# Kernel tuning notes

Hardware: AMD Instinct MI355X
Metric: run time of the kernel (lower is better)

The kernel has to match this reference:

```python
import jax, jax.numpy as jnp
import numpy as np

N_NODES = 100000
N_EDGES = 600000
H = 128


def setup_inputs() -> dict:
    key = jax.random.key(0)
    k_z, k_e, k_w1, k_w2 = jax.random.split(key, 4)
    z = jax.random.normal(k_z, (N_NODES, H), dtype=jnp.float32)
    edge_index = jax.random.randint(k_e, (2, N_EDGES), 0, N_NODES, dtype=jnp.int64)
    # Kaiming-ish init scale for the MLP weights
    W1 = jax.random.normal(k_w1, (2 * H, H), dtype=jnp.float32) * (1.0 / np.sqrt(2 * H))
    b1 = jnp.zeros((H,), dtype=jnp.float32)
    W2 = jax.random.normal(k_w2, (H, 1), dtype=jnp.float32) * (1.0 / np.sqrt(H))
    b2 = jnp.zeros((1,), dtype=jnp.float32)
    return {"z": z, "edge_index": edge_index, "W1": W1, "b1": b1, "W2": W2, "b2": b2}


def reference(z, edge_index, W1, b1, W2, b2):
    # Gather source/destination node embeddings: [E, H] each
    src = z[edge_index[0]]
    dst = z[edge_index[1]]
    # Avoid materializing the [E, 2H] concat: split W1 into src/dst blocks
    # so fc1(cat(src,dst)) == src @ W1[:H] + dst @ W1[H:] + b1
    h = src @ W1[:H] + dst @ W1[H:] + b1  # [E, H]
    h = jax.nn.relu(h)
    out = h @ W2 + b2  # [E, 1]
    return out.reshape(-1)
```

## Files before the change

### kernel.cpp

```cpp
#include <hip/hip_runtime.h>
#include <hip/hip_bf16.h>
#include <stdint.h>

#define N_NODES_C 100000
#define N_EDGES_C 600000
#define H_C 128

typedef __bf16 bf16x8 __attribute__((ext_vector_type(8)));
typedef float f32x16 __attribute__((ext_vector_type(16)));
typedef float f32x4v __attribute__((ext_vector_type(4)));
typedef _Float16 half8 __attribute__((ext_vector_type(8)));
typedef unsigned short ushort8 __attribute__((ext_vector_type(8)));

#define LDS_STRIDE 136

__device__ __forceinline__ unsigned short f2bf(float f) {
    unsigned int u = __builtin_bit_cast(unsigned int, f);
    u += 0x7fffu + ((u >> 16) & 1u);
    return (unsigned short)(u >> 16);
}

__global__ void w1fmt_kernel(const float* __restrict__ W1,
                             unsigned short* __restrict__ w1f) {
    int i = blockIdx.x * blockDim.x + threadIdx.x;
    if (i >= 8 * 8 * 64 * 8) return;
    int j = i & 7;
    int L = (i >> 3) & 63;
    int t = (i >> 9) & 7;
    int s = (i >> 12) & 7;
    int k  = s * 16 + ((L >> 5) * 8) + j;
    int n2 = t * 32 + (L & 31);
    float w = (n2 < 128) ? W1[k * H_C + n2]
                         : W1[(128 + k) * H_C + (n2 - 128)];
    w1f[i] = f2bf(w);
}

__launch_bounds__(256, 2)
__global__ void node_gemm_kernel(const float* __restrict__ z,
                                 const unsigned short* __restrict__ w1f,
                                 const float* __restrict__ b1,
                                 _Float16* __restrict__ uv) {
    __shared__ unsigned short smem[32 * LDS_STRIDE];

    const int lane = threadIdx.x & 63;
    const int wv   = threadIdx.x >> 6;
    const int l31  = lane & 31;
    const int half = lane >> 5;
    const int uh   = wv >> 1;
    const int tile = blockIdx.x;

    {
        const int sr = threadIdx.x >> 3;
        const int sc = (threadIdx.x & 7) * 16;
        const float* src = z + (size_t)(tile * 32 + sr) * H_C + sc;
        f32x4v f0 = *reinterpret_cast<const f32x4v*>(src);
        f32x4v f1 = *reinterpret_cast<const f32x4v*>(src + 4);
        f32x4v f2 = *reinterpret_cast<const f32x4v*>(src + 8);
        f32x4v f3 = *reinterpret_cast<const f32x4v*>(src + 12);
        ushort8 lo, hi;
        #pragma unroll
        for (int j = 0; j < 4; ++j) {
            lo[j]     = f2bf(f0[j]);
            lo[j + 4] = f2bf(f1[j]);
            hi[j]     = f2bf(f2[j]);
            hi[j + 4] = f2bf(f3[j]);
        }
        *reinterpret_cast<ushort8*>(smem + sr * LDS_STRIDE + sc)     = lo;
        *reinterpret_cast<ushort8*>(smem + sr * LDS_STRIDE + sc + 8) = hi;
    }

    bf16x8 bfrag[8][2];
    #pragma unroll
    for (int s = 0; s < 8; ++s) {
        #pragma unroll
        for (int t = 0; t < 2; ++t) {
            bfrag[s][t] = reinterpret_cast<const bf16x8*>(w1f)
                              [(s * 8 + wv * 2 + t) * 64 + lane];
        }
    }

    float badd[2];
    int   ncol[2];
    #pragma unroll
    for (int t = 0; t < 2; ++t) {
        int n2  = (wv * 2 + t) * 32 + l31;
        ncol[t] = n2 - uh * 128;
        badd[t] = uh ? 0.0f : b1[n2];
    }
    const size_t segbase = uh ? (size_t)N_NODES_C * H_C : 0;

    __syncthreads();

    f32x16 acc[2] = {};
    #pragma unroll
    for (int s = 0; s < 8; ++s) {
        bf16x8 a = *reinterpret_cast<const bf16x8*>(
                       smem + l31 * LDS_STRIDE + s * 16 + half * 8);
        acc[0] = __builtin_amdgcn_mfma_f32_32x32x16_bf16(a, bfrag[s][0], acc[0], 0, 0, 0);
        acc[1] = __builtin_amdgcn_mfma_f32_32x32x16_bf16(a, bfrag[s][1], acc[1], 0, 0, 0);
    }

    const int node0 = tile * 32;
    #pragma unroll
    for (int t = 0; t < 2; ++t) {
        #pragma unroll
        for (int r = 0; r < 16; ++r) {
            int row = (r & 3) + 8 * (r >> 2) + 4 * half;
            float v = acc[t][r] + badd[t];
            float fo = __shfl_xor(v, 1);
            if ((lane & 1) == 0) {
                unsigned int pk = __builtin_bit_cast(
                    unsigned int, __builtin_amdgcn_cvt_pkrtz(v, fo));
                size_t idx = segbase + (size_t)(node0 + row) * H_C + ncol[t];
                *reinterpret_cast<unsigned int*>(uv + idx) = pk;
            }
        }
    }
}

__global__ void edge_kernel(const _Float16* __restrict__ uv,
                            const int* __restrict__ ei,
                            const float* __restrict__ w2,
                            const float* __restrict__ b2,
                            float* __restrict__ out) {
    const int tid = blockIdx.x * blockDim.x + threadIdx.x;
    const int j   = tid & 15;
    const int q   = tid >> 4;
    const int e0  = q * 8;
    if (e0 >= N_EDGES_C) return;

    float w2v[8];
    {
        f32x4v a = *reinterpret_cast<const f32x4v*>(w2 + j * 8);
        f32x4v b = *reinterpret_cast<const f32x4v*>(w2 + j * 8 + 4);
        #pragma unroll
        for (int k = 0; k < 4; ++k) { w2v[k] = a[k]; w2v[k + 4] = b[k]; }
    }
    const float c2 = b2[0];
    const _Float16* vbase = uv + (size_t)N_NODES_C * H_C;

    int4 sa = *reinterpret_cast<const int4*>(ei + e0);
    int4 sb = *reinterpret_cast<const int4*>(ei + e0 + 4);
    int4 da = *reinterpret_cast<const int4*>(ei + N_EDGES_C + e0);
    int4 db = *reinterpret_cast<const int4*>(ei + N_EDGES_C + e0 + 4);

    int se[8] = { sa.x, sa.y, sa.z, sa.w, sb.x, sb.y, sb.z, sb.w };
    int de[8] = { da.x, da.y, da.z, da.w, db.x, db.y, db.z, db.w };

    half8 uu[8], vv[8];
    #pragma unroll
    for (int i = 0; i < 8; ++i) {
        uu[i] = *reinterpret_cast<const half8*>(uv    + (size_t)se[i] * H_C + j * 8);
        vv[i] = *reinterpret_cast<const half8*>(vbase + (size_t)de[i] * H_C + j * 8);
    }

    float p[8];
    #pragma unroll
    for (int i = 0; i < 8; ++i) {
        float acc = 0.0f;
        #pragma unroll
        for (int k = 0; k < 8; ++k) {
            float h = (float)uu[i][k] + (float)vv[i][k];
            h = h > 0.0f ? h : 0.0f;
            acc = fmaf(h, w2v[k], acc);
        }
        p[i] = acc;
    }
    #pragma unroll
    for (int m = 1; m <= 8; m <<= 1) {
        #pragma unroll
        for (int i = 0; i < 8; ++i) p[i] += __shfl_xor(p[i], m);
    }
    if (j == 0) {
        float4 o0 = { p[0] + c2, p[1] + c2, p[2] + c2, p[3] + c2 };
        float4 o1 = { p[4] + c2, p[5] + c2, p[6] + c2, p[7] + c2 };
        *reinterpret_cast<float4*>(out + e0)     = o0;
        *reinterpret_cast<float4*>(out + e0 + 4) = o1;
    }
}

extern "C" void kernel_launch(void* const* d_in, const int* in_sizes, int n_in,
                              void* d_out, int out_size, void* d_ws, size_t ws_size,
                              hipStream_t stream) {
    const float* z  = (const float*)d_in[0];
    const int*   ei = (const int*)d_in[1];
    const float* W1 = (const float*)d_in[2];
    const float* b1 = (const float*)d_in[3];
    const float* W2 = (const float*)d_in[4];
    const float* b2 = (const float*)d_in[5];
    float* out = (float*)d_out;

    unsigned short* w1f = (unsigned short*)d_ws;
    _Float16* uv = (_Float16*)((char*)d_ws + 65536);

    w1fmt_kernel<<<(8 * 8 * 64 * 8 + 255) / 256, 256, 0, stream>>>(W1, w1f);

    node_gemm_kernel<<<N_NODES_C / 32, 256, 0, stream>>>(z, w1f, b1, uv);

    int nquarters = N_EDGES_C / 8;
    edge_kernel<<<(nquarters * 16 + 255) / 256, 256, 0, stream>>>(uv, ei, W2, b2, out);
}
```

Baseline: 151.0 us.

## Make node GEMM persistent with double-buffered LDS and register prefetch of z

The node GEMM kernel now runs a fixed grid of 512 blocks that loop over tiles in a grid-stride fashion. It loads the W1 fragments into registers once per block rather than once per tile. It prefetches the next tile's z rows into registers while the current tile's MFMAs and stores run, and writes them into a second LDS buffer. This amortises the weight loads and hides global load latency, at the cost of more registers and lower parallelism per tile.

After: 151.2 us. No clear change (+0.1%).

```diff
diff --git a/kernel.cpp b/kernel.cpp
--- a/kernel.cpp
+++ b/kernel.cpp
@@ -13,6 +13,7 @@
 typedef unsigned short ushort8 __attribute__((ext_vector_type(8)));
 
 #define LDS_STRIDE 136
+#define NODE_GRID 512
 
 __device__ __forceinline__ unsigned short f2bf(float f) {
     unsigned int u = __builtin_bit_cast(unsigned int, f);
@@ -40,18 +41,41 @@
                                  const unsigned short* __restrict__ w1f,
                                  const float* __restrict__ b1,
                                  _Float16* __restrict__ uv) {
-    __shared__ unsigned short smem[32 * LDS_STRIDE];
+    __shared__ unsigned short smem[2][32 * LDS_STRIDE];
 
     const int lane = threadIdx.x & 63;
     const int wv   = threadIdx.x >> 6;
     const int l31  = lane & 31;
     const int half = lane >> 5;
     const int uh   = wv >> 1;
-    const int tile = blockIdx.x;
+
+    const int sr = threadIdx.x >> 3;
+    const int sc = (threadIdx.x & 7) * 16;
+
+    bf16x8 bfrag[8][2];
+    #pragma unroll
+    for (int s = 0; s < 8; ++s) {
+        #pragma unroll
+        for (int t = 0; t < 2; ++t) {
+            bfrag[s][t] = reinterpret_cast<const bf16x8*>(w1f)
+                              [(s * 8 + wv * 2 + t) * 64 + lane];
+        }
+    }
+    float badd[2];
+    int   ncol[2];
+    #pragma unroll
+    for (int t = 0; t < 2; ++t) {
+        int n2  = (wv * 2 + t) * 32 + l31;
+        ncol[t] = n2 - uh * 128;
+        badd[t] = uh ? 0.0f : b1[n2];
+    }
+    const size_t segbase = uh ? (size_t)N_NODES_C * H_C : 0;
+
+    const int NT = N_NODES_C / 32;
+    int tile = blockIdx.x;
+    if (tile >= NT) return;
 
     {
-        const int sr = threadIdx.x >> 3;
-        const int sc = (threadIdx.x & 7) * 16;
         const float* src = z + (size_t)(tile * 32 + sr) * H_C + sc;
         f32x4v f0 = *reinterpret_cast<const f32x4v*>(src);
         f32x4v f1 = *reinterpret_cast<const f32x4v*>(src + 4);
@@ -60,61 +84,78 @@
         ushort8 lo, hi;
         #pragma unroll
         for (int j = 0; j < 4; ++j) {
-            lo[j]     = f2bf(f0[j]);
-            lo[j + 4] = f2bf(f1[j]);
-            hi[j]     = f2bf(f2[j]);
-            hi[j + 4] = f2bf(f3[j]);
-        }
-        *reinterpret_cast<ushort8*>(smem + sr * LDS_STRIDE + sc)     = lo;
-        *reinterpret_cast<ushort8*>(smem + sr * LDS_STRIDE + sc + 8) = hi;
-    }
-
-    bf16x8 bfrag[8][2];
-    #pragma unroll
-    for (int s = 0; s < 8; ++s) {
+            lo[j] = f2bf(f0[j]); lo[j + 4] = f2bf(f1[j]);
+            hi[j] = f2bf(f2[j]); hi[j + 4] = f2bf(f3[j]);
+        }
+        *reinterpret_cast<ushort8*>(smem[0] + sr * LDS_STRIDE + sc)     = lo;
+        *reinterpret_cast<ushort8*>(smem[0] + sr * LDS_STRIDE + sc + 8) = hi;
+    }
+
+    int  nxt     = tile + NODE_GRID;
+    bool has_nxt = (nxt < NT);
+    f32x4v g0, g1, g2, g3;
+    if (has_nxt) {
+        const float* src = z + (size_t)(nxt * 32 + sr) * H_C + sc;
+        g0 = *reinterpret_cast<const f32x4v*>(src);
+        g1 = *reinterpret_cast<const f32x4v*>(src + 4);
+        g2 = *reinterpret_cast<const f32x4v*>(src + 8);
+        g3 = *reinterpret_cast<const f32x4v*>(src + 12);
+    }
+    __syncthreads();
+
+    int buf = 0;
+    for (;;) {
+        f32x16 acc[2] = {};
+        #pragma unroll
+        for (int s = 0; s < 8; ++s) {
+            bf16x8 a = *reinterpret_cast<const bf16x8*>(
+                           smem[buf] + l31 * LDS_STRIDE + s * 16 + half * 8);
+            acc[0] = __builtin_amdgcn_mfma_f32_32x32x16_bf16(a, bfrag[s][0], acc[0], 0, 0, 0);
+            acc[1] = __builtin_amdgcn_mfma_f32_32x32x16_bf16(a, bfrag[s][1], acc[1], 0, 0, 0);
+        }
+
+        const int node0 = tile * 32;
         #pragma unroll
         for (int t = 0; t < 2; ++t) {
-            bfrag[s][t] = reinterpret_cast<const bf16x8*>(w1f)
-                              [(s * 8 + wv * 2 + t) * 64 + lane];
-        }
-    }
-
-    float badd[2];
-    int   ncol[2];
-    #pragma unroll
-    for (int t = 0; t < 2; ++t) {
-        int n2  = (wv * 2 + t) * 32 + l31;
-        ncol[t] = n2 - uh * 128;
-        badd[t] = uh ? 0.0f : b1[n2];
-    }
-    const size_t segbase = uh ? (size_t)N_NODES_C * H_C : 0;
-
-    __syncthreads();
-
-    f32x16 acc[2] = {};
-    #pragma unroll
-    for (int s = 0; s < 8; ++s) {
-        bf16x8 a = *reinterpret_cast<const bf16x8*>(
-                       smem + l31 * LDS_STRIDE + s * 16 + half * 8);
-        acc[0] = __builtin_amdgcn_mfma_f32_32x32x16_bf16(a, bfrag[s][0], acc[0], 0, 0, 0);
-        acc[1] = __builtin_amdgcn_mfma_f32_32x32x16_bf16(a, bfrag[s][1], acc[1], 0, 0, 0);
-    }
-
-    const int node0 = tile * 32;
-    #pragma unroll
-    for (int t = 0; t < 2; ++t) {
-        #pragma unroll
-        for (int r = 0; r < 16; ++r) {
-            int row = (r & 3) + 8 * (r >> 2) + 4 * half;
-            float v = acc[t][r] + badd[t];
-            float fo = __shfl_xor(v, 1);
-            if ((lane & 1) == 0) {
-                unsigned int pk = __builtin_bit_cast(
-                    unsigned int, __builtin_amdgcn_cvt_pkrtz(v, fo));
-                size_t idx = segbase + (size_t)(node0 + row) * H_C + ncol[t];
-                *reinterpret_cast<unsigned int*>(uv + idx) = pk;
+            #pragma unroll
+            for (int r = 0; r < 16; ++r) {
+                int row = (r & 3) + 8 * (r >> 2) + 4 * half;
+                float v = acc[t][r] + badd[t];
+                float fo = __shfl_xor(v, 1);
+                if ((lane & 1) == 0) {
+                    unsigned int pk = __builtin_bit_cast(
+                        unsigned int, __builtin_amdgcn_cvt_pkrtz(v, fo));
+                    size_t idx = segbase + (size_t)(node0 + row) * H_C + ncol[t];
+                    *reinterpret_cast<unsigned int*>(uv + idx) = pk;
+                }
             }
         }
+
+        if (!has_nxt) break;
+
+        {
+            ushort8 lo, hi;
+            #pragma unroll
+            for (int j = 0; j < 4; ++j) {
+                lo[j] = f2bf(g0[j]); lo[j + 4] = f2bf(g1[j]);
+                hi[j] = f2bf(g2[j]); hi[j + 4] = f2bf(g3[j]);
+            }
+            *reinterpret_cast<ushort8*>(smem[1 - buf] + sr * LDS_STRIDE + sc)     = lo;
+            *reinterpret_cast<ushort8*>(smem[1 - buf] + sr * LDS_STRIDE + sc + 8) = hi;
+        }
+
+        tile = nxt;
+        nxt += NODE_GRID;
+        has_nxt = (nxt < NT);
+        if (has_nxt) {
+            const float* src = z + (size_t)(nxt * 32 + sr) * H_C + sc;
+            g0 = *reinterpret_cast<const f32x4v*>(src);
+            g1 = *reinterpret_cast<const f32x4v*>(src + 4);
+            g2 = *reinterpret_cast<const f32x4v*>(src + 8);
+            g3 = *reinterpret_cast<const f32x4v*>(src + 12);
+        }
+        __syncthreads();
+        buf ^= 1;
     }
 }
 
@@ -195,7 +236,7 @@
 
     w1fmt_kernel<<<(8 * 8 * 64 * 8 + 255) / 256, 256, 0, stream>>>(W1, w1f);
 
-    node_gemm_kernel<<<N_NODES_C / 32, 256, 0, stream>>>(z, w1f, b1, uv);
+    node_gemm_kernel<<<NODE_GRID, 256, 0, stream>>>(z, w1f, b1, uv);
 
     int nquarters = N_EDGES_C / 8;
     edge_kernel<<<(nquarters * 16 + 255) / 256, 256, 0, stream>>>(uv, ei, W2, b2, out);
```
